# Optimization experiments

Measured on AMD Instinct MI355X. Metric: run time of the kernel, lower is better.

## Reference

```python
import jax, jax.numpy as jnp
import numpy as np

B, T, F, A = 4096, 200, 64, 128
H = 100        # LSTM / dense hidden size (hard-coded in module)
OUT = 10       # output_size


def setup_inputs() -> dict:
    key = jax.random.key(0)
    ks = jax.random.split(key, 14)
    s = 0.05  # small init so the relu-activated LSTM doesn't explode over T=200 steps
    return {
        "attributes": jax.random.normal(ks[0], (B, A), jnp.float32),
        "sequences": jax.random.normal(ks[1], (B, T, F), jnp.float32),
        # Dense(100) on attributes
        "Wd": jax.random.normal(ks[2], (A, H), jnp.float32) * s,
        "bd": jnp.zeros((H,), jnp.float32),
        # LSTM(100, activation='relu'): kernel, recurrent_kernel, bias (keras gate order i,f,c,o)
        "Wk": jax.random.normal(ks[3], (F, 4 * H), jnp.float32) * s,
        "Wr": jax.random.normal(ks[4], (H, 4 * H), jnp.float32) * s,
        "bl": jnp.zeros((4 * H,), jnp.float32),
        # process_1: Dense(100) on concat [B, 2H]
        "W1": jax.random.normal(ks[5], (2 * H, H), jnp.float32) * s,
        "b1": jnp.zeros((H,), jnp.float32),
        # process_2: Dense(50)
        "W2": jax.random.normal(ks[6], (H, 50), jnp.float32) * s,
        "b2": jnp.zeros((50,), jnp.float32),
        # classify: Dense(OUT, softmax)
        "Wc": jax.random.normal(ks[7], (50, OUT), jnp.float32) * s,
        "bc": jnp.zeros((OUT,), jnp.float32),
    }


def _lstm_relu(sequences, Wk, Wr, bl):
    # keras LSTM with activation='relu', recurrent_activation=sigmoid (default).
    # Pre-project all timesteps with the input kernel (one big GEMM),
    # then scan the small recurrent update.
    x_proj = jnp.einsum('btf,fg->btg', sequences, Wk) + bl  # [B, T, 4H]
    h0 = jnp.zeros((sequences.shape[0], H), sequences.dtype)
    c0 = jnp.zeros_like(h0)

    def step(carry, xt):
        h, c = carry
        z = xt + h @ Wr                      # [B, 4H]
        zi, zf, zg, zo = jnp.split(z, 4, axis=-1)  # keras gate order: i, f, c(g), o
        i = jax.nn.sigmoid(zi)
        f = jax.nn.sigmoid(zf)
        g = jax.nn.relu(zg)                  # activation='relu'
        o = jax.nn.sigmoid(zo)
        c = f * c + i * g
        h = o * jax.nn.relu(c)               # activation='relu' on cell output too
        return (h, c), None

    (h, _), _ = jax.lax.scan(step, (h0, c0), x_proj.transpose(1, 0, 2))
    return h  # [B, H] (return_sequences=False -> last hidden state)


def reference(attributes, sequences, Wd, bd, Wk, Wr, bl, W1, b1, W2, b2, Wc, bc):
    attr = jax.nn.relu(attributes @ Wd + bd)          # Dense(100, relu)
    long = _lstm_relu(sequences, Wk, Wr, bl)          # LSTM(100, relu)
    x = jnp.concatenate([attr, long], axis=1)         # [B, 2H]
    x = jax.nn.relu(x @ W1 + b1)                      # process_1
    x = jax.nn.relu(x @ W2 + b2)                      # process_2
    return jax.nn.softmax(x @ Wc + bc, axis=-1)       # classify
```

## Files before the change

kernel.cpp:

```cpp
#include <hip/hip_runtime.h>
#include <hip/hip_bf16.h>

#define T_LEN 200
#define F_IN 64
#define A_IN 128
#define H 100
#define H4 400
#define OUT_N 10
#define ROWS 16

typedef __attribute__((ext_vector_type(8))) short bf16x8;
typedef __attribute__((ext_vector_type(4))) float f32x4;

__device__ __forceinline__ unsigned short f2bf(float f) {
    union { float f; unsigned u; } v; v.f = f;
    unsigned r = v.u + 0x7FFFu + ((v.u >> 16) & 1u);
    return (unsigned short)(r >> 16);
}

__device__ __forceinline__ unsigned cvtpk(float lo, float hi) {
    unsigned r;
    asm("v_cvt_pk_bf16_f32 %0, %1, %2" : "=v"(r) : "v"(lo), "v"(hi));
    return r;
}

__device__ __forceinline__ float sigm(float x) {
    return 1.0f / (1.0f + __expf(-x));
}

#define HOFF(b, j) ((((j) >> 5) * 64 + ((b) + 16 * (((j) >> 3) & 3))) * 8 + ((j) & 7))

extern "C" __global__ void __launch_bounds__(512, 2)
traj_kernel(const float* __restrict__ attrs, const float* __restrict__ seq,
            const float* __restrict__ Wd, const float* __restrict__ bd,
            const float* __restrict__ Wk, const float* __restrict__ Wr,
            const float* __restrict__ bl, const float* __restrict__ W1,
            const float* __restrict__ b1, const float* __restrict__ W2,
            const float* __restrict__ b2, const float* __restrict__ Wc,
            const float* __restrict__ bc, float* __restrict__ out)
{
    __shared__ __align__(16) char smem[27648];
    unsigned short* hl = (unsigned short*)smem;
    float* h32 = (float*)(smem + 8192);

    const int tid = threadIdx.x;
    const int lane = tid & 63;
    const int w = tid >> 6;
    const int ln15 = lane & 15;
    const int lg = lane >> 4;
    const int b0 = blockIdx.x * ROWS;

    const int nt0 = 3 * w;
    const int ntc = (w == 7) ? 4 : 3;
    const bool w7 = (w == 7);

    bf16x8 wkf[4][2];
    bf16x8 wrf[4][4];
    f32x4 blf[4];
    const int rw = ln15 & 3;
    const int qr = ln15 >> 2;
#pragma unroll
    for (int q = 0; q < 4; q++) {
        const bool v = (q < ntc);
        const int tile = nt0 + q;
        const int c = v ? (tile * 4 + qr) + 100 * rw : 0;
#pragma unroll
        for (int kt = 0; kt < 2; kt++) {
            bf16x8 f;
#pragma unroll
            for (int i = 0; i < 8; i++) {
                int k = kt * 32 + lg * 8 + i;
                f[i] = (short)f2bf(v ? Wk[k * H4 + c] : 0.0f);
            }
            wkf[q][kt] = f;
        }
#pragma unroll
        for (int kt = 0; kt < 4; kt++) {
            bf16x8 f;
#pragma unroll
            for (int i = 0; i < 8; i++) {
                int k = kt * 32 + lg * 8 + i;
                f[i] = (short)f2bf((v && k < H) ? Wr[k * H4 + c] : 0.0f);
            }
            wrf[q][kt] = f;
        }
        int j = tile * 4 + lg;
        if (v) blf[q] = (f32x4){ bl[j], bl[H + j], bl[2 * H + j], bl[3 * H + j] };
        else   blf[q] = (f32x4){ 0.f, 0.f, 0.f, 0.f };
    }

    int hoq[4], h32q[4];
#pragma unroll
    for (int q = 0; q < 4; q++) {
        int j = (nt0 + q) * 4 + lg;
        if (j > 99) j = 99;
        hoq[q] = HOFF(ln15, j);
        h32q[q] = ln15 * H + j;
    }
    float cr0 = 0.f, cr1 = 0.f, cr2 = 0.f, cr3 = 0.f;

    for (int i = tid; i < 4096; i += 512) hl[i] = 0;

    const float* sp = seq + (size_t)(b0 + ln15) * (T_LEN * F_IN) + lg * 8;
    f32x4 s0 = *(const f32x4*)(sp);
    f32x4 s1 = *(const f32x4*)(sp + 4);
    f32x4 s2 = *(const f32x4*)(sp + 32);
    f32x4 s3 = *(const f32x4*)(sp + 36);
    sp += F_IN;

    f32x4 accX[4];
    {
        union { unsigned u[4]; bf16x8 v; } ua, ub;
        ua.u[0] = cvtpk(s0[0], s0[1]); ua.u[1] = cvtpk(s0[2], s0[3]);
        ua.u[2] = cvtpk(s1[0], s1[1]); ua.u[3] = cvtpk(s1[2], s1[3]);
        ub.u[0] = cvtpk(s2[0], s2[1]); ub.u[1] = cvtpk(s2[2], s2[3]);
        ub.u[2] = cvtpk(s3[0], s3[1]); ub.u[3] = cvtpk(s3[2], s3[3]);
        bf16x8 a0 = ua.v, a1 = ub.v;
#pragma unroll
        for (int q = 0; q < 3; q++) {
            f32x4 x = __builtin_amdgcn_mfma_f32_16x16x32_bf16(wkf[q][0], a0, blf[q], 0, 0, 0);
            accX[q] = __builtin_amdgcn_mfma_f32_16x16x32_bf16(wkf[q][1], a1, x, 0, 0, 0);
        }
        if (w7) {
            f32x4 x = __builtin_amdgcn_mfma_f32_16x16x32_bf16(wkf[3][0], a0, blf[3], 0, 0, 0);
            accX[3] = __builtin_amdgcn_mfma_f32_16x16x32_bf16(wkf[3][1], a1, x, 0, 0, 0);
        }
    }
    s0 = *(const f32x4*)(sp);
    s1 = *(const f32x4*)(sp + 4);
    s2 = *(const f32x4*)(sp + 32);
    s3 = *(const f32x4*)(sp + 36);
    sp += F_IN;

    __syncthreads();

    for (int t = 0; t < T_LEN; t++) {
        const bool notlast = (t < T_LEN - 1);
        const bool last = !notlast;

        const unsigned short* hp = hl + ((t & 1) << 11) + lane * 8;
        bf16x8 hf0 = *(const bf16x8*)(hp);
        bf16x8 hf1 = *(const bf16x8*)(hp + 512);
        bf16x8 hf2 = *(const bf16x8*)(hp + 1024);
        bf16x8 hf3 = *(const bf16x8*)(hp + 1536);

        bf16x8 a0n = {}, a1n = {};
        if (notlast) {
            union { unsigned u[4]; bf16x8 v; } ua, ub;
            ua.u[0] = cvtpk(s0[0], s0[1]); ua.u[1] = cvtpk(s0[2], s0[3]);
            ua.u[2] = cvtpk(s1[0], s1[1]); ua.u[3] = cvtpk(s1[2], s1[3]);
            ub.u[0] = cvtpk(s2[0], s2[1]); ub.u[1] = cvtpk(s2[2], s2[3]);
            ub.u[2] = cvtpk(s3[0], s3[1]); ub.u[3] = cvtpk(s3[2], s3[3]);
            a0n = ua.v; a1n = ub.v;
        }

        f32x4 rr[4];
#pragma unroll
        for (int q = 0; q < 3; q++)
            rr[q] = __builtin_amdgcn_mfma_f32_16x16x32_bf16(wrf[q][0], hf0, accX[q], 0, 0, 0);
        if (w7)
            rr[3] = __builtin_amdgcn_mfma_f32_16x16x32_bf16(wrf[3][0], hf0, accX[3], 0, 0, 0);
#pragma unroll
        for (int q = 0; q < 3; q++)
            rr[q] = __builtin_amdgcn_mfma_f32_16x16x32_bf16(wrf[q][1], hf1, rr[q], 0, 0, 0);
        if (w7)
            rr[3] = __builtin_amdgcn_mfma_f32_16x16x32_bf16(wrf[3][1], hf1, rr[3], 0, 0, 0);
#pragma unroll
        for (int q = 0; q < 3; q++)
            rr[q] = __builtin_amdgcn_mfma_f32_16x16x32_bf16(wrf[q][2], hf2, rr[q], 0, 0, 0);
        if (w7)
            rr[3] = __builtin_amdgcn_mfma_f32_16x16x32_bf16(wrf[3][2], hf2, rr[3], 0, 0, 0);
#pragma unroll
        for (int q = 0; q < 3; q++)
            rr[q] = __builtin_amdgcn_mfma_f32_16x16x32_bf16(wrf[q][3], hf3, rr[q], 0, 0, 0);
        if (w7)
            rr[3] = __builtin_amdgcn_mfma_f32_16x16x32_bf16(wrf[3][3], hf3, rr[3], 0, 0, 0);

        if (t < T_LEN - 2) {
            s0 = *(const f32x4*)(sp);
            s1 = *(const f32x4*)(sp + 4);
            s2 = *(const f32x4*)(sp + 32);
            s3 = *(const f32x4*)(sp + 36);
            sp += F_IN;
        }

        unsigned short* hwp = hl + (((t + 1) & 1) << 11);

#define DOGATE(RRQ, CR, HO, HW) do {                                  \
            float _i = sigm(RRQ[0]), _f = sigm(RRQ[1]);               \
            float _g = fmaxf(RRQ[2], 0.0f), _o = sigm(RRQ[3]);        \
            CR = _f * CR + _i * _g;                                   \
            float _h = _o * fmaxf(CR, 0.0f);                          \
            hwp[HO] = (unsigned short)cvtpk(_h, _h);                  \
            if (last) h32[HW] = _h;                                   \
        } while (0)

        DOGATE(rr[0], cr0, hoq[0], h32q[0]);
        DOGATE(rr[1], cr1, hoq[1], h32q[1]);
        DOGATE(rr[2], cr2, hoq[2], h32q[2]);
        if (w7) DOGATE(rr[3], cr3, hoq[3], h32q[3]);

        if (notlast) {
#pragma unroll
            for (int q = 0; q < 3; q++) {
                f32x4 x = __builtin_amdgcn_mfma_f32_16x16x32_bf16(wkf[q][0], a0n, blf[q], 0, 0, 0);
                accX[q] = __builtin_amdgcn_mfma_f32_16x16x32_bf16(wkf[q][1], a1n, x, 0, 0, 0);
            }
            if (w7) {
                f32x4 x = __builtin_amdgcn_mfma_f32_16x16x32_bf16(wkf[3][0], a0n, blf[3], 0, 0, 0);
                accX[3] = __builtin_amdgcn_mfma_f32_16x16x32_bf16(wkf[3][1], a1n, x, 0, 0, 0);
            }
        }

        __syncthreads();
    }

    float* att  = (float*)smem;
    float* catb = (float*)(smem + 14592);
    float* x1b  = (float*)smem;
    float* x2b  = (float*)(smem + 8192);
    float* lgb  = (float*)(smem + 11392);

    {
        const f32x4* src = (const f32x4*)(attrs + (size_t)b0 * A_IN);
        ((f32x4*)att)[tid] = src[tid];
    }
    __syncthreads();

#pragma unroll
    for (int k = 0; k < 4; k++) {
        int e = tid + 512 * k;
        if (e < ROWS * H) {
            int b = e & 15, j = e >> 4;
            float s = bd[j];
            for (int kk = 0; kk < A_IN; kk++) s += att[b * A_IN + kk] * Wd[kk * H + j];
            catb[b * 200 + j] = fmaxf(s, 0.0f);
            catb[b * 200 + H + j] = h32[b * H + j];
        }
    }
    __syncthreads();

#pragma unroll
    for (int k = 0; k < 4; k++) {
        int e = tid + 512 * k;
        if (e < ROWS * H) {
            int b = e & 15, j = e >> 4;
            float s = b1[j];
            for (int kk = 0; kk < 200; kk++) s += catb[b * 200 + kk] * W1[kk * H + j];
            x1b[b * H + j] = fmaxf(s, 0.0f);
        }
    }
    __syncthreads();

#pragma unroll
    for (int k = 0; k < 2; k++) {
        int e = tid + 512 * k;
        if (e < ROWS * 50) {
            int b = e & 15, j = e >> 4;
            float s = b2[j];
            for (int kk = 0; kk < H; kk++) s += x1b[b * H + kk] * W2[kk * 50 + j];
            x2b[b * 50 + j] = fmaxf(s, 0.0f);
        }
    }
    __syncthreads();

    if (tid < ROWS * OUT_N) {
        int b = tid / OUT_N, o = tid % OUT_N;
        float s = bc[o];
        for (int kk = 0; kk < 50; kk++) s += x2b[b * 50 + kk] * Wc[kk * OUT_N + o];
        lgb[b * OUT_N + o] = s;
    }
    __syncthreads();

    if (tid < ROWS) {
        int b = tid;
        float m = -1e30f, v[10];
#pragma unroll
        for (int o = 0; o < 10; o++) { v[o] = lgb[b * 10 + o]; m = fmaxf(m, v[o]); }
        float ssum = 0.0f;
#pragma unroll
        for (int o = 0; o < 10; o++) { v[o] = __expf(v[o] - m); ssum += v[o]; }
        float inv = 1.0f / ssum;
#pragma unroll
        for (int o = 0; o < 10; o++) out[(size_t)(b0 + b) * 10 + o] = v[o] * inv;
    }
}

extern "C" void kernel_launch(void* const* d_in, const int* in_sizes, int n_in,
                              void* d_out, int out_size, void* d_ws, size_t ws_size,
                              hipStream_t stream) {
    const float* attrs = (const float*)d_in[0];
    const float* seq   = (const float*)d_in[1];
    const float* Wd    = (const float*)d_in[2];
    const float* bd    = (const float*)d_in[3];
    const float* Wk    = (const float*)d_in[4];
    const float* Wr    = (const float*)d_in[5];
    const float* bl    = (const float*)d_in[6];
    const float* W1    = (const float*)d_in[7];
    const float* b1    = (const float*)d_in[8];
    const float* W2    = (const float*)d_in[9];
    const float* b2    = (const float*)d_in[10];
    const float* Wc    = (const float*)d_in[11];
    const float* bc    = (const float*)d_in[12];
    float* out = (float*)d_out;

    hipLaunchKernelGGL(traj_kernel, dim3(256), dim3(512), 0, stream,
                       attrs, seq, Wd, bd, Wk, Wr, bl, W1, b1, W2, b2, Wc, bc, out);
}
```

Baseline: 285.8 us.

## Fold gate scaling and bias into weights, use exp2/rcp sigmoid, lighten barriers

Pre-scales the i/f/o gate columns of the input and recurrent weights by -log2(e), so the sigmoid becomes a raw exp2 plus a hardware reciprocal. The LSTM bias is folded into the recurrent weights through a constant-1 entry in padded row k=100 of the hidden state, which removes the bias registers and the per-step bias accumulation. The per-step __syncthreads is replaced by an LDS waitcnt plus s_barrier, MFMA issue is wrapped in s_setprio, and the final hidden state is kept in registers and written once after the loop instead of under a per-step branch. This trades bf16 rounding of the bias and scaled weights, plus the approximate exp2/rcp, for fewer ALU ops and a lighter barrier in the serial recurrence.

Result: faster. 246.4 us (-13.8%).

```diff
diff --git a/kernel.cpp b/kernel.cpp
--- a/kernel.cpp
+++ b/kernel.cpp
@@ -12,6 +12,8 @@
 typedef __attribute__((ext_vector_type(8))) short bf16x8;
 typedef __attribute__((ext_vector_type(4))) float f32x4;
 
+#define NLOG2E -1.4426950408889634f
+
 __device__ __forceinline__ unsigned short f2bf(float f) {
     union { float f; unsigned u; } v; v.f = f;
     unsigned r = v.u + 0x7FFFu + ((v.u >> 16) & 1u);
@@ -24,8 +26,13 @@
     return r;
 }
 
-__device__ __forceinline__ float sigm(float x) {
-    return 1.0f / (1.0f + __expf(-x));
+__device__ __forceinline__ float sigm2(float zp) {
+    return __builtin_amdgcn_rcpf(1.0f + __builtin_amdgcn_exp2f(zp));
+}
+
+__device__ __forceinline__ void lds_barrier() {
+    asm volatile("s_waitcnt lgkmcnt(0)" ::: "memory");
+    __builtin_amdgcn_s_barrier();
 }
 
 #define HOFF(b, j) ((((j) >> 5) * 64 + ((b) + 16 * (((j) >> 3) & 3))) * 8 + ((j) & 7))
@@ -54,52 +61,63 @@
     const int ntc = (w == 7) ? 4 : 3;
     const bool w7 = (w == 7);
 
-    bf16x8 wkf[4][2];
-    bf16x8 wrf[4][4];
-    f32x4 blf[4];
     const int rw = ln15 & 3;
     const int qr = ln15 >> 2;
+    const float gsc = (rw == 2) ? 1.0f : NLOG2E;
+
+    bf16x8 wkf[4][2];
 #pragma unroll
     for (int q = 0; q < 4; q++) {
         const bool v = (q < ntc);
-        const int tile = nt0 + q;
-        const int c = v ? (tile * 4 + qr) + 100 * rw : 0;
+        const int c = v ? ((nt0 + q) * 4 + qr) + 100 * rw : 0;
 #pragma unroll
         for (int kt = 0; kt < 2; kt++) {
             bf16x8 f;
 #pragma unroll
             for (int i = 0; i < 8; i++) {
                 int k = kt * 32 + lg * 8 + i;
-                f[i] = (short)f2bf(v ? Wk[k * H4 + c] : 0.0f);
+                f[i] = (short)f2bf(v ? gsc * Wk[k * H4 + c] : 0.0f);
             }
             wkf[q][kt] = f;
         }
+    }
+
+    bf16x8 wrf[4][4];
+#pragma unroll
+    for (int q = 0; q < 4; q++) {
+        const bool v = (q < ntc);
+        const int c = v ? ((nt0 + q) * 4 + qr) + 100 * rw : 0;
 #pragma unroll
         for (int kt = 0; kt < 4; kt++) {
             bf16x8 f;
 #pragma unroll
             for (int i = 0; i < 8; i++) {
                 int k = kt * 32 + lg * 8 + i;
-                f[i] = (short)f2bf((v && k < H) ? Wr[k * H4 + c] : 0.0f);
+                float x = 0.0f;
+                if (v && k < H) x = gsc * Wr[k * H4 + c];
+                if (v && k == H) x = gsc * bl[c];
+                f[i] = (short)f2bf(x);
             }
             wrf[q][kt] = f;
         }
-        int j = tile * 4 + lg;
-        if (v) blf[q] = (f32x4){ bl[j], bl[H + j], bl[2 * H + j], bl[3 * H + j] };
-        else   blf[q] = (f32x4){ 0.f, 0.f, 0.f, 0.f };
-    }
-
-    int hoq[4], h32q[4];
+    }
+
+    int hoq[4];
 #pragma unroll
     for (int q = 0; q < 4; q++) {
         int j = (nt0 + q) * 4 + lg;
         if (j > 99) j = 99;
         hoq[q] = HOFF(ln15, j);
-        h32q[q] = ln15 * H + j;
     }
     float cr0 = 0.f, cr1 = 0.f, cr2 = 0.f, cr3 = 0.f;
+    float hq0 = 0.f, hq1 = 0.f, hq2 = 0.f, hq3 = 0.f;
 
     for (int i = tid; i < 4096; i += 512) hl[i] = 0;
+    __syncthreads();
+    if (tid < 32) {
+        int b = tid & 15, buf = tid >> 4;
+        hl[buf * 2048 + 1536 + 8 * b + 4] = 0x3F80;
+    }
 
     const float* sp = seq + (size_t)(b0 + ln15) * (T_LEN * F_IN) + lg * 8;
     f32x4 s0 = *(const f32x4*)(sp);
@@ -116,13 +134,14 @@
         ub.u[0] = cvtpk(s2[0], s2[1]); ub.u[1] = cvtpk(s2[2], s2[3]);
         ub.u[2] = cvtpk(s3[0], s3[1]); ub.u[3] = cvtpk(s3[2], s3[3]);
         bf16x8 a0 = ua.v, a1 = ub.v;
+        const f32x4 zz = { 0.f, 0.f, 0.f, 0.f };
 #pragma unroll
         for (int q = 0; q < 3; q++) {
-            f32x4 x = __builtin_amdgcn_mfma_f32_16x16x32_bf16(wkf[q][0], a0, blf[q], 0, 0, 0);
+            f32x4 x = __builtin_amdgcn_mfma_f32_16x16x32_bf16(wkf[q][0], a0, zz, 0, 0, 0);
             accX[q] = __builtin_amdgcn_mfma_f32_16x16x32_bf16(wkf[q][1], a1, x, 0, 0, 0);
         }
         if (w7) {
-            f32x4 x = __builtin_amdgcn_mfma_f32_16x16x32_bf16(wkf[3][0], a0, blf[3], 0, 0, 0);
+            f32x4 x = __builtin_amdgcn_mfma_f32_16x16x32_bf16(wkf[3][0], a0, zz, 0, 0, 0);
             accX[3] = __builtin_amdgcn_mfma_f32_16x16x32_bf16(wkf[3][1], a1, x, 0, 0, 0);
         }
     }
@@ -132,11 +151,10 @@
     s3 = *(const f32x4*)(sp + 36);
     sp += F_IN;
 
-    __syncthreads();
+    lds_barrier();
 
     for (int t = 0; t < T_LEN; t++) {
         const bool notlast = (t < T_LEN - 1);
-        const bool last = !notlast;
 
         const unsigned short* hp = hl + ((t & 1) << 11) + lane * 8;
         bf16x8 hf0 = *(const bf16x8*)(hp);
@@ -155,6 +173,7 @@
         }
 
         f32x4 rr[4];
+        __builtin_amdgcn_s_setprio(1);
 #pragma unroll
         for (int q = 0; q < 3; q++)
             rr[q] = __builtin_amdgcn_mfma_f32_16x16x32_bf16(wrf[q][0], hf0, accX[q], 0, 0, 0);
@@ -175,6 +194,7 @@
             rr[q] = __builtin_amdgcn_mfma_f32_16x16x32_bf16(wrf[q][3], hf3, rr[q], 0, 0, 0);
         if (w7)
             rr[3] = __builtin_amdgcn_mfma_f32_16x16x32_bf16(wrf[3][3], hf3, rr[3], 0, 0, 0);
+        __builtin_amdgcn_s_setprio(0);
 
         if (t < T_LEN - 2) {
             s0 = *(const f32x4*)(sp);
@@ -186,34 +206,40 @@
 
         unsigned short* hwp = hl + (((t + 1) & 1) << 11);
 
-#define DOGATE(RRQ, CR, HO, HW) do {                                  \
-            float _i = sigm(RRQ[0]), _f = sigm(RRQ[1]);               \
-            float _g = fmaxf(RRQ[2], 0.0f), _o = sigm(RRQ[3]);        \
-            CR = _f * CR + _i * _g;                                   \
-            float _h = _o * fmaxf(CR, 0.0f);                          \
-            hwp[HO] = (unsigned short)cvtpk(_h, _h);                  \
-            if (last) h32[HW] = _h;                                   \
+#define DOGATE(RRQ, CR, HQ, Q) do {                                    \
+            float _i = sigm2(RRQ[0]), _f = sigm2(RRQ[1]);              \
+            float _g = fmaxf(RRQ[2], 0.0f), _o = sigm2(RRQ[3]);        \
+            CR = _f * CR + _i * _g;                                    \
+            float _h = _o * fmaxf(CR, 0.0f);                           \
+            HQ = _h;                                                   \
+            hwp[hoq[Q]] = (unsigned short)cvtpk(_h, _h);               \
         } while (0)
 
-        DOGATE(rr[0], cr0, hoq[0], h32q[0]);
-        DOGATE(rr[1], cr1, hoq[1], h32q[1]);
-        DOGATE(rr[2], cr2, hoq[2], h32q[2]);
-        if (w7) DOGATE(rr[3], cr3, hoq[3], h32q[3]);
+        DOGATE(rr[0], cr0, hq0, 0);
+        DOGATE(rr[1], cr1, hq1, 1);
+        DOGATE(rr[2], cr2, hq2, 2);
+        if (w7) DOGATE(rr[3], cr3, hq3, 3);
 
         if (notlast) {
+            const f32x4 zz = { 0.f, 0.f, 0.f, 0.f };
 #pragma unroll
             for (int q = 0; q < 3; q++) {
-                f32x4 x = __builtin_amdgcn_mfma_f32_16x16x32_bf16(wkf[q][0], a0n, blf[q], 0, 0, 0);
+                f32x4 x = __builtin_amdgcn_mfma_f32_16x16x32_bf16(wkf[q][0], a0n, zz, 0, 0, 0);
                 accX[q] = __builtin_amdgcn_mfma_f32_16x16x32_bf16(wkf[q][1], a1n, x, 0, 0, 0);
             }
             if (w7) {
-                f32x4 x = __builtin_amdgcn_mfma_f32_16x16x32_bf16(wkf[3][0], a0n, blf[3], 0, 0, 0);
+                f32x4 x = __builtin_amdgcn_mfma_f32_16x16x32_bf16(wkf[3][0], a0n, zz, 0, 0, 0);
                 accX[3] = __builtin_amdgcn_mfma_f32_16x16x32_bf16(wkf[3][1], a1n, x, 0, 0, 0);
             }
         }
 
-        __syncthreads();
-    }
+        lds_barrier();
+    }
+
+#pragma unroll
+    for (int q = 0; q < 3; q++)
+        h32[ln15 * H + (nt0 + q) * 4 + lg] = (q == 0) ? hq0 : (q == 1) ? hq1 : hq2;
+    if (w7) h32[ln15 * H + 24 * 4 + lg] = hq3;
 
     float* att  = (float*)smem;
     float* catb = (float*)(smem + 14592);
@@ -223,7 +249,9 @@
 
     {
         const f32x4* src = (const f32x4*)(attrs + (size_t)b0 * A_IN);
-        ((f32x4*)att)[tid] = src[tid];
+        f32x4 v = src[tid];
+        __syncthreads();
+        ((f32x4*)att)[tid] = v;
     }
     __syncthreads();
 
```
